# Optimization experiments

Measured on AMD Instinct MI355X. Metric: run time of the kernel, lower is better.

The kernel has to match this reference:

```python
import jax, jax.numpy as jnp
import numpy as np
from jax import lax

K = 3  # kernel size
PAD = K // 2


def _patches(x):
    # x: [B,C,H,W] -> [B,C,K*K,H,W] (zero-padded 'same' neighborhoods)
    B, C, H, W = x.shape
    xp = jnp.pad(x, ((0, 0), (0, 0), (PAD, PAD), (PAD, PAD)))
    ps = [xp[:, :, i:i + H, j:j + W] for i in range(K) for j in range(K)]
    return jnp.stack(ps, axis=2)


def pac_conv2d(x, guide, w, b):
    # Pixel-adaptive conv (pacnet, kernel_type='gaussian', not channel-wise).
    # adaptive kernel from guidance: exp(-0.5 * ||g_patch - g_center||^2)
    gp = _patches(guide)                      # [B,C,P,H,W]
    d2 = jnp.sum((gp - guide[:, :, None]) ** 2, axis=1)  # [B,P,H,W]
    kern = jnp.exp(-0.5 * d2)                 # [B,P,H,W]
    xp = _patches(x)                          # [B,Cin,P,H,W]
    wf = w.reshape(w.shape[0], w.shape[1], K * K)  # [Cout,Cin,P]
    out = jnp.einsum('bcphw,bphw,ocp->bohw', xp, kern, wf)
    return out + b[None, :, None, None]


def conv2d(x, w, b):
    out = lax.conv_general_dilated(x, w, (1, 1), 'SAME',
                                   dimension_numbers=('NCHW', 'OIHW', 'NCHW'))
    return out + b[None, :, None, None]


def setup_inputs() -> dict:
    key = jax.random.key(0)
    ks = jax.random.split(key, 10)
    B, C, H, W = 8, 64, 128, 128
    fan = C * K * K
    s = 1.0 / np.sqrt(fan)
    inp = {
        'x': jax.random.normal(ks[0], (B, C, H, W), jnp.float32),
        'edge': jax.random.normal(ks[1], (B, C, H, W), jnp.float32),
        'w_pac1': jax.random.normal(ks[2], (C, C, K, K), jnp.float32) * s,
        'b_pac1': jax.random.normal(ks[3], (C,), jnp.float32) * s,
        'w_pac2': jax.random.normal(ks[4], (C, C, K, K), jnp.float32) * s,
        'b_pac2': jax.random.normal(ks[5], (C,), jnp.float32) * s,
        'w_e1': jax.random.normal(ks[6], (C, C, K, K), jnp.float32) * s,
        'b_e1': jax.random.normal(ks[7], (C,), jnp.float32) * s,
        'w_e2': jax.random.normal(ks[8], (C, C, K, K), jnp.float32) * s,
        'b_e2': jax.random.normal(ks[9], (C,), jnp.float32) * s,
    }
    return inp


def reference(x, edge, w_pac1, b_pac1, w_pac2, b_pac2, w_e1, b_e1, w_e2, b_e2):
    res_scale = 1.0
    # i=0: pac conv on sr (guided by current edge), plain conv on edge
    res_sr = pac_conv2d(x, edge, w_pac1, b_pac1)
    res_edge = conv2d(edge, w_e1, b_e1)
    # i=1: activation on both
    res_sr = jax.nn.relu(res_sr)
    res_edge = jax.nn.relu(res_edge)
    # i=2: pac conv guided by updated edge, plain conv on edge
    res_sr = pac_conv2d(res_sr, res_edge, w_pac2, b_pac2)
    res_edge = conv2d(res_edge, w_e2, b_e2)
    # dual residual
    res_sr = x + res_sr * res_scale
    res_edge = edge + res_edge * res_scale
    return (res_sr, res_edge)
```

## Files before the change

kernel.cpp:

```cpp
#include <hip/hip_runtime.h>

typedef unsigned short u16;
typedef __attribute__((ext_vector_type(8))) short s8;
typedef __attribute__((ext_vector_type(4))) float f4;

#define B_  8
#define C_  64
#define H_  128
#define W_  128
#define HW_ (H_*W_)
#define PITCH 72
#define WSZ 36864


static __device__ __forceinline__ u16 f2bu(float f) {
    union { float f; unsigned u; } c; c.f = f;
    unsigned u = c.u;
    u += 0x7fffu + ((u >> 16) & 1u);
    return (u16)(u >> 16);
}
static __device__ __forceinline__ float bu2f(u16 u) {
    union { unsigned u; float f; } c; c.u = ((unsigned)u) << 16; return c.f;
}

__global__ __launch_bounds__(256) void wt_all(
    const float* __restrict__ w0, const float* __restrict__ w1,
    const float* __restrict__ w2, const float* __restrict__ w3,
    u16* __restrict__ dst)
{
    int idx = blockIdx.x*256 + threadIdx.x;
    int cid = blockIdx.y;
    const float* w = (cid == 0) ? w0 : (cid == 1) ? w1 : (cid == 2) ? w2 : w3;
    int p = idx >> 12, o = (idx >> 6) & 63, c = idx & 63;
    dst[(size_t)cid*WSZ + idx] = f2bu(w[((size_t)o*64 + c)*9 + p]);
}

static __device__ __forceinline__ void stage_tile(
    u16* __restrict__ s_t, const u16* __restrict__ src, int b, int th0, int tw0, int t)
{
    for (int i = t; i < 10*18*8; i += 256) {
        int pix = i >> 3, ch = i & 7;
        int rr = pix / 18, ww = pix - rr*18;
        int gr = th0 + rr - 1, gw = tw0 + ww - 1;
        uint4 v = {0u,0u,0u,0u};
        if ((unsigned)gr < (unsigned)H_ && (unsigned)gw < (unsigned)W_)
            v = *(const uint4*)(src + ((size_t)b*HW_ + gr*W_ + gw)*64 + ch*8);
        *(uint4*)(&s_t[pix*PITCH + ch*8]) = v;
    }
}

static __device__ __forceinline__ void stage_tile_f32(
    u16* __restrict__ s_t, const float* __restrict__ src, int b, int th0, int tw0, int t)
{
    const bool lok = (tw0 != 0);
    const bool rok = (tw0 != W_ - 16);
    for (int i = t; i < 320; i += 256) {
        const int cp = i & 31, rr = i >> 5;
        const int gr = th0 + rr - 1;
        const int c0 = cp * 2;
        float v0[18], v1[18];
        if ((unsigned)gr < (unsigned)H_) {
            const float* a0 = src + ((size_t)b*C_ + c0)*HW_ + (size_t)gr*W_ + tw0;
            const float* a1 = a0 + HW_;
            v0[0]  = lok ? a0[-1] : 0.f;
            v1[0]  = lok ? a1[-1] : 0.f;
#pragma unroll
            for (int g = 0; g < 4; ++g) {
                *(f4*)(v0 + 1 + g*4) = *(const f4*)(a0 + g*4);
                *(f4*)(v1 + 1 + g*4) = *(const f4*)(a1 + g*4);
            }
            v0[17] = rok ? a0[16] : 0.f;
            v1[17] = rok ? a1[16] : 0.f;
        } else {
#pragma unroll
            for (int j = 0; j < 18; ++j) { v0[j] = 0.f; v1[j] = 0.f; }
        }
#pragma unroll
        for (int j = 0; j < 18; ++j) {
            unsigned pk = (unsigned)f2bu(v0[j]) | ((unsigned)f2bu(v1[j]) << 16);
            *(unsigned*)(&s_t[(rr*18 + j)*PITCH + c0]) = pk;
        }
    }
}

template<bool PAC>
static __device__ __forceinline__ void conv_core(
    const u16* __restrict__ s_t, const float* __restrict__ s_k,
    const u16* __restrict__ w, const float* __restrict__ bias,
    f4 acc[2][4], int wvM, int wvN, int ln, int quad)
{
#pragma unroll
    for (int mf = 0; mf < 2; ++mf) {
        f4 bv;
#pragma unroll
        for (int r = 0; r < 4; ++r) bv[r] = bias[wvM*32 + mf*16 + quad*4 + r];
#pragma unroll
        for (int nf = 0; nf < 4; ++nf) acc[mf][nf] = bv;
    }

#pragma unroll
    for (int p = 0; p < 9; ++p) {
        const int dr = p / 3, dc = p - dr*3;
        s8 a[2][2];
#pragma unroll
        for (int mf = 0; mf < 2; ++mf)
#pragma unroll
            for (int kc = 0; kc < 2; ++kc)
                a[mf][kc] = *(const s8*)(w + (((size_t)p*64 + wvM*32 + mf*16 + ln)*64 + kc*32 + quad*8));
        s8 bfr[4][2];
#pragma unroll
        for (int nf = 0; nf < 4; ++nf) {
            const u16* base = &s_t[((wvN*4 + nf + dr)*18 + ln + dc)*PITCH];
#pragma unroll
            for (int kc = 0; kc < 2; ++kc)
                bfr[nf][kc] = *(const s8*)(base + kc*32 + quad*8);
        }
        if (PAC) {
            float kv[4];
#pragma unroll
            for (int nf = 0; nf < 4; ++nf)
                kv[nf] = s_k[p*128 + (wvN*4 + nf)*16 + ln];
#pragma unroll
            for (int mf = 0; mf < 2; ++mf)
#pragma unroll
                for (int nf = 0; nf < 4; ++nf) {
                    f4 d = {0.f, 0.f, 0.f, 0.f};
                    d = __builtin_amdgcn_mfma_f32_16x16x32_bf16(a[mf][0], bfr[nf][0], d, 0, 0, 0);
                    d = __builtin_amdgcn_mfma_f32_16x16x32_bf16(a[mf][1], bfr[nf][1], d, 0, 0, 0);
                    acc[mf][nf] += kv[nf] * d;
                }
        } else {
#pragma unroll
            for (int mf = 0; mf < 2; ++mf)
#pragma unroll
                for (int nf = 0; nf < 4; ++nf) {
                    acc[mf][nf] = __builtin_amdgcn_mfma_f32_16x16x32_bf16(a[mf][0], bfr[nf][0], acc[mf][nf], 0, 0, 0);
                    acc[mf][nf] = __builtin_amdgcn_mfma_f32_16x16x32_bf16(a[mf][1], bfr[nf][1], acc[mf][nf], 0, 0, 0);
                }
        }
    }
}

static __device__ __forceinline__ void store_t(
    u16* __restrict__ out, f4 acc[2][4], int b, int th0, int tw0,
    int wvM, int wvN, int ln, int quad)
{
#pragma unroll
    for (int mf = 0; mf < 2; ++mf)
#pragma unroll
        for (int nf = 0; nf < 4; ++nf) {
            f4 v = acc[mf][nf];
            ushort4 o;
            o.x = f2bu(fmaxf(v[0], 0.f)); o.y = f2bu(fmaxf(v[1], 0.f));
            o.z = f2bu(fmaxf(v[2], 0.f)); o.w = f2bu(fmaxf(v[3], 0.f));
            size_t pix = (size_t)b*HW_ + (th0 + wvN*4 + nf)*W_ + tw0 + ln;
            *(ushort4*)(out + pix*64 + wvM*32 + mf*16 + quad*4) = o;
        }
}

static __device__ __forceinline__ void store_f(
    float* __restrict__ out, const float* __restrict__ resid,
    f4 acc[2][4], int b, int th0, int tw0, int wvM, int wvN, int ln, int quad)
{
#pragma unroll
    for (int mf = 0; mf < 2; ++mf)
#pragma unroll
        for (int nf = 0; nf < 4; ++nf) {
#pragma unroll
            for (int r = 0; r < 4; ++r) {
                int och = wvM*32 + mf*16 + quad*4 + r;
                size_t idx = ((size_t)b*C_ + och)*HW_ + (th0 + wvN*4 + nf)*W_ + tw0 + ln;
                out[idx] = acc[mf][nf][r] + resid[idx];
            }
        }
}

template<bool STAGE1>
__global__ __launch_bounds__(256, 2) void fused_stage(
    const float* __restrict__ inA_f, const float* __restrict__ inB_f,
    const u16* __restrict__ inA_t, const u16* __restrict__ inB_t,
    const u16* __restrict__ wA, const u16* __restrict__ wB,
    const float* __restrict__ biasA, const float* __restrict__ biasB,
    const float* __restrict__ residA_f, const float* __restrict__ residB_f,
    u16* __restrict__ outA_t, u16* __restrict__ outB_t,
    float* __restrict__ outA_f, float* __restrict__ outB_f)
{
    __shared__ u16   s_t[10*18*PITCH];
    __shared__ float s_k[9*128];

    const int t    = threadIdx.x;
    const int L    = blockIdx.x;
    const int b    = L & 7;
    const int tw0  = ((L >> 3) & 7) * 16;
    const int th0  = (L >> 6) * 8;
    const int wv   = t >> 6;
    const int wvM  = wv >> 1;
    const int wvN  = wv & 1;
    const int lane = t & 63;
    const int ln   = lane & 15;
    const int quad = lane >> 4;

    if (STAGE1) stage_tile_f32(s_t, inA_f, b, th0, tw0, t);
    else        stage_tile    (s_t, inA_t, b, th0, tw0, t);
    __syncthreads();

    {
        const int px   = t & 127;
        const int half = t >> 7;
        const int p0   = half ? 5 : 0;
        const int np   = half ? 4 : 5;
        const int py   = px >> 4, pxc = px & 15;
        float d2[5];
#pragma unroll
        for (int k = 0; k < 5; ++k) d2[k] = 0.f;
        const u16* cb = &s_t[((py+1)*18 + (pxc+1))*PITCH];
#pragma unroll 1
        for (int co = 0; co < 8; ++co) {
            s8 c8 = *(const s8*)(cb + co*8);
            float cf[8];
#pragma unroll
            for (int j = 0; j < 8; ++j) cf[j] = bu2f((u16)c8[j]);
#pragma unroll
            for (int k = 0; k < 5; ++k) {
                if (k < np) {
                    int p = p0 + k;
                    int dr = p / 3, dc = p - dr*3;
                    s8 n8 = *(const s8*)(&s_t[((py + dr)*18 + pxc + dc)*PITCH + co*8]);
#pragma unroll
                    for (int j = 0; j < 8; ++j) {
                        float d = bu2f((u16)n8[j]) - cf[j];
                        d2[k] += d * d;
                    }
                }
            }
        }
#pragma unroll
        for (int k = 0; k < 5; ++k)
            if (k < np) s_k[(p0+k)*128 + px] = __expf(-0.5f * d2[k]);
    }

    {
        f4 acc[2][4];
        conv_core<false>(s_t, nullptr, wA, biasA, acc, wvM, wvN, ln, quad);
        if (STAGE1) store_t(outA_t, acc, b, th0, tw0, wvM, wvN, ln, quad);
        else        store_f(outA_f, residA_f, acc, b, th0, tw0, wvM, wvN, ln, quad);
    }

    __syncthreads();
    if (STAGE1) stage_tile_f32(s_t, inB_f, b, th0, tw0, t);
    else        stage_tile    (s_t, inB_t, b, th0, tw0, t);
    __syncthreads();

    {
        f4 acc[2][4];
        conv_core<true>(s_t, s_k, wB, biasB, acc, wvM, wvN, ln, quad);
        if (STAGE1) store_t(outB_t, acc, b, th0, tw0, wvM, wvN, ln, quad);
        else        store_f(outB_f, residB_f, acc, b, th0, tw0, wvM, wvN, ln, quad);
    }
}

extern "C" void kernel_launch(void* const* d_in, const int* in_sizes, int n_in,
                              void* d_out, int out_size, void* d_ws, size_t ws_size,
                              hipStream_t stream)
{
    const float* x      = (const float*)d_in[0];
    const float* edge   = (const float*)d_in[1];
    const float* w_pac1 = (const float*)d_in[2];
    const float* b_pac1 = (const float*)d_in[3];
    const float* w_pac2 = (const float*)d_in[4];
    const float* b_pac2 = (const float*)d_in[5];
    const float* w_e1   = (const float*)d_in[6];
    const float* b_e1   = (const float*)d_in[7];
    const float* w_e2   = (const float*)d_in[8];
    const float* b_e2   = (const float*)d_in[9];

    float* out_sr   = (float*)d_out;
    float* out_edge = out_sr + (size_t)B_*C_*HW_;

    const size_t NT = (size_t)B_*HW_*64;
    u16* res_edge1_t = (u16*)d_ws;
    u16* res_sr1_t   = res_edge1_t + NT;
    u16* w_t         = res_sr1_t + NT;

    dim3 blk(256);

    wt_all<<<dim3(144, 4), blk, 0, stream>>>(w_e1, w_pac1, w_e2, w_pac2, w_t);

    fused_stage<true ><<<dim3(1024), blk, 0, stream>>>(
        edge, x, nullptr, nullptr,
        w_t + 0*WSZ, w_t + 1*WSZ, b_e1, b_pac1,
        nullptr, nullptr, res_edge1_t, res_sr1_t, nullptr, nullptr);
    fused_stage<false><<<dim3(1024), blk, 0, stream>>>(
        nullptr, nullptr, res_edge1_t, res_sr1_t,
        w_t + 2*WSZ, w_t + 3*WSZ, b_e2, b_pac2,
        edge, x, nullptr, nullptr, out_edge, out_sr);
}
```

Before: 231.2 us.

## Merge weight transform and both stages into one cooperative persistent kernel

Replaces three kernel launches (weight transform, stage 1, stage 2) with a single cooperative kernel that uses grid-wide syncs between phases. The aim is to remove launch gaps and tail effects between kernels. Cooperative launch needs all 1024 blocks co-resident (4 per CU on 256 CUs), so the code checks occupancy and falls back to the old path otherwise. Grid syncs add barrier cost, and the occupancy requirement may not be met with launch_bounds(256,2) hints.

```diff
diff --git a/kernel.cpp b/kernel.cpp
--- a/kernel.cpp
+++ b/kernel.cpp
@@ -1,4 +1,5 @@
 #include <hip/hip_runtime.h>
+#include <hip/hip_cooperative_groups.h>
 
 typedef unsigned short u16;
 typedef __attribute__((ext_vector_type(8))) short s8;
@@ -176,18 +177,16 @@
 }
 
 template<bool STAGE1>
-__global__ __launch_bounds__(256, 2) void fused_stage(
+static __device__ __forceinline__ void phase_body(
     const float* __restrict__ inA_f, const float* __restrict__ inB_f,
     const u16* __restrict__ inA_t, const u16* __restrict__ inB_t,
     const u16* __restrict__ wA, const u16* __restrict__ wB,
     const float* __restrict__ biasA, const float* __restrict__ biasB,
     const float* __restrict__ residA_f, const float* __restrict__ residB_f,
     u16* __restrict__ outA_t, u16* __restrict__ outB_t,
-    float* __restrict__ outA_f, float* __restrict__ outB_f)
-{
-    __shared__ u16   s_t[10*18*PITCH];
-    __shared__ float s_k[9*128];
-
+    float* __restrict__ outA_f, float* __restrict__ outB_f,
+    u16* __restrict__ s_t, float* __restrict__ s_k)
+{
     const int t    = threadIdx.x;
     const int L    = blockIdx.x;
     const int b    = L & 7;
@@ -259,6 +258,63 @@
     }
 }
 
+template<bool STAGE1>
+__global__ __launch_bounds__(256, 2) void fused_stage(
+    const float* __restrict__ inA_f, const float* __restrict__ inB_f,
+    const u16* __restrict__ inA_t, const u16* __restrict__ inB_t,
+    const u16* __restrict__ wA, const u16* __restrict__ wB,
+    const float* __restrict__ biasA, const float* __restrict__ biasB,
+    const float* __restrict__ residA_f, const float* __restrict__ residB_f,
+    u16* __restrict__ outA_t, u16* __restrict__ outB_t,
+    float* __restrict__ outA_f, float* __restrict__ outB_f)
+{
+    __shared__ u16   s_t[10*18*PITCH];
+    __shared__ float s_k[9*128];
+    phase_body<STAGE1>(inA_f, inB_f, inA_t, inB_t, wA, wB, biasA, biasB,
+                       residA_f, residB_f, outA_t, outB_t, outA_f, outB_f, s_t, s_k);
+}
+
+__global__ __launch_bounds__(256, 2) void fused_all(
+    const float* __restrict__ x, const float* __restrict__ edge,
+    const float* __restrict__ w_pac1, const float* __restrict__ b_pac1,
+    const float* __restrict__ w_pac2, const float* __restrict__ b_pac2,
+    const float* __restrict__ w_e1,  const float* __restrict__ b_e1,
+    const float* __restrict__ w_e2,  const float* __restrict__ b_e2,
+    u16* __restrict__ res_edge1_t, u16* __restrict__ res_sr1_t,
+    u16* __restrict__ w_t, float* __restrict__ out_sr, float* __restrict__ out_edge)
+{
+    __shared__ u16   s_t[10*18*PITCH];
+    __shared__ float s_k[9*128];
+
+    cooperative_groups::grid_group grid = cooperative_groups::this_grid();
+
+    {
+        int gid = blockIdx.x*256 + threadIdx.x;
+        if (gid < 4*WSZ) {
+            int cid = gid / WSZ;
+            int idx = gid - cid*WSZ;
+            const float* w = (cid == 0) ? w_e1 : (cid == 1) ? w_pac1
+                           : (cid == 2) ? w_e2 : w_pac2;
+            int p = idx >> 12, o = (idx >> 6) & 63, c = idx & 63;
+            w_t[(size_t)cid*WSZ + idx] = f2bu(w[((size_t)o*64 + c)*9 + p]);
+        }
+    }
+    __threadfence();
+    grid.sync();
+
+    phase_body<true>(edge, x, nullptr, nullptr,
+                     w_t + 0*WSZ, w_t + 1*WSZ, b_e1, b_pac1,
+                     nullptr, nullptr, res_edge1_t, res_sr1_t, nullptr, nullptr,
+                     s_t, s_k);
+    __threadfence();
+    grid.sync();
+
+    phase_body<false>(nullptr, nullptr, res_edge1_t, res_sr1_t,
+                      w_t + 2*WSZ, w_t + 3*WSZ, b_e2, b_pac2,
+                      edge, x, nullptr, nullptr, out_edge, out_sr,
+                      s_t, s_k);
+}
+
 extern "C" void kernel_launch(void* const* d_in, const int* in_sizes, int n_in,
                               void* d_out, int out_size, void* d_ws, size_t ws_size,
                               hipStream_t stream)
@@ -282,16 +338,33 @@
     u16* res_sr1_t   = res_edge1_t + NT;
     u16* w_t         = res_sr1_t + NT;
 
-    dim3 blk(256);
-
-    wt_all<<<dim3(144, 4), blk, 0, stream>>>(w_e1, w_pac1, w_e2, w_pac2, w_t);
-
-    fused_stage<true ><<<dim3(1024), blk, 0, stream>>>(
-        edge, x, nullptr, nullptr,
-        w_t + 0*WSZ, w_t + 1*WSZ, b_e1, b_pac1,
-        nullptr, nullptr, res_edge1_t, res_sr1_t, nullptr, nullptr);
-    fused_stage<false><<<dim3(1024), blk, 0, stream>>>(
-        nullptr, nullptr, res_edge1_t, res_sr1_t,
-        w_t + 2*WSZ, w_t + 3*WSZ, b_e2, b_pac2,
-        edge, x, nullptr, nullptr, out_edge, out_sr);
-}
+    static int coop_ok = -1;
+    if (coop_ok < 0) {
+        int nb = 0;
+        hipError_t e = hipOccupancyMaxActiveBlocksPerMultiprocessor(
+            &nb, reinterpret_cast<const void*>(&fused_all), 256, 0);
+        coop_ok = (e == hipSuccess && nb >= 4) ? 1 : 0;
+    }
+
+    if (coop_ok) {
+        void* args[] = {
+            (void*)&x, (void*)&edge,
+            (void*)&w_pac1, (void*)&b_pac1, (void*)&w_pac2, (void*)&b_pac2,
+            (void*)&w_e1,  (void*)&b_e1,  (void*)&w_e2,  (void*)&b_e2,
+            (void*)&res_edge1_t, (void*)&res_sr1_t, (void*)&w_t,
+            (void*)&out_sr, (void*)&out_edge
+        };
+        hipLaunchCooperativeKernel(reinterpret_cast<const void*>(&fused_all),
+                                   dim3(1024), dim3(256), args, 0, stream);
+    } else {
+        wt_all<<<dim3(144, 4), dim3(256), 0, stream>>>(w_e1, w_pac1, w_e2, w_pac2, w_t);
+        fused_stage<true ><<<dim3(1024), dim3(256), 0, stream>>>(
+            edge, x, nullptr, nullptr,
+            w_t + 0*WSZ, w_t + 1*WSZ, b_e1, b_pac1,
+            nullptr, nullptr, res_edge1_t, res_sr1_t, nullptr, nullptr);
+        fused_stage<false><<<dim3(1024), dim3(256), 0, stream>>>(
+            nullptr, nullptr, res_edge1_t, res_sr1_t,
+            w_t + 2*WSZ, w_t + 3*WSZ, b_e2, b_pac2,
+            edge, x, nullptr, nullptr, out_edge, out_sr);
+    }
+}
```

Result: faster. 222.0 us (-4.0%).
